# Kernel optimization log

Hardware: AMD Instinct MI355X
Metric: run time of the kernel (lower is better)

## Reference

```python
import jax, jax.numpy as jnp
import numpy as np
from jax import lax

LATENT = 128
CODEBOOK = 1024

def _conv(x, w, b):
    # NCHW conv, kernel OIHW, stride 1, padding 1 (same)
    y = lax.conv_general_dilated(x, w, (1, 1), ((1, 1), (1, 1)),
                                 dimension_numbers=('NCHW', 'OIHW', 'NCHW'))
    return y + b[None, :, None, None]

def _conv_transpose(x, w, b):
    # ConvTranspose2d(k=3, s=1, p=1) == conv with flipped kernel, in/out swapped, pad 1
    w_eff = jnp.flip(w, (2, 3)).transpose(1, 0, 2, 3)  # [Cin,Cout,3,3] -> [Cout,Cin,3,3]
    return _conv(x, w_eff, b)

def _maxpool2(x):
    return lax.reduce_window(x, -jnp.inf, lax.max, (1, 1, 2, 2), (1, 1, 2, 2), 'VALID')

def _upsample2(x):
    # F.interpolate(scale_factor=2), default nearest
    return jnp.repeat(jnp.repeat(x, 2, axis=2), 2, axis=3)

def setup_inputs() -> dict:
    key = jax.random.key(0)
    ks = jax.random.split(key, 20)
    f = jnp.float32
    inp = {
        'x': jax.random.uniform(ks[0], (8192, 1, 24, 24), dtype=f),
        'conv1_w': jax.random.normal(ks[1], (32, 1, 3, 3), f) * 0.1,
        'conv1_b': jnp.zeros((32,), f),
        'conv2_w': jax.random.normal(ks[2], (64, 32, 3, 3), f) * 0.05,
        'conv2_b': jnp.zeros((64,), f),
        'conv3_w': jax.random.normal(ks[3], (128, 64, 3, 3), f) * 0.04,
        'conv3_b': jnp.zeros((128,), f),
        'enc_fc_w': jax.random.normal(ks[4], (LATENT, 3 * 3 * 128), f) * 0.03,
        'enc_fc_b': jnp.zeros((LATENT,), f),
        'codebook': jax.random.normal(ks[5], (CODEBOOK, LATENT), f),
        'dec_fc_w': jax.random.normal(ks[6], (3 * 3 * 128, LATENT), f) * 0.09,
        'dec_fc_b': jnp.zeros((3 * 3 * 128,), f),
        'dct1_w': jax.random.normal(ks[7], (128, 64, 3, 3), f) * 0.03,  # [Cin,Cout,kh,kw]
        'dct1_b': jnp.zeros((64,), f),
        'dct2_w': jax.random.normal(ks[8], (64, 32, 3, 3), f) * 0.04,
        'dct2_b': jnp.zeros((32,), f),
        'dct3_w': jax.random.normal(ks[9], (32, 1, 3, 3), f) * 0.06,
        'dct3_b': jnp.zeros((1,), f),
    }
    return inp

def reference(x, conv1_w, conv1_b, conv2_w, conv2_b, conv3_w, conv3_b,
              enc_fc_w, enc_fc_b, codebook, dec_fc_w, dec_fc_b,
              dct1_w, dct1_b, dct2_w, dct2_b, dct3_w, dct3_b):
    # ---- Encoder ----
    h = _maxpool2(jax.nn.relu(_conv(x, conv1_w, conv1_b)))     # [B,32,12,12]
    h = _maxpool2(jax.nn.relu(_conv(h, conv2_w, conv2_b)))     # [B,64,6,6]
    h = _maxpool2(jax.nn.relu(_conv(h, conv3_w, conv3_b)))     # [B,128,3,3]
    z = h.reshape(-1, 3 * 3 * 128) @ enc_fc_w.T + enc_fc_b     # [B,128]
    # ---- Quantize (L2 nearest-codeword; matmul-trick distances, same argmin) ----
    d2 = (jnp.sum(z * z, axis=1, keepdims=True)
          - 2.0 * z @ codebook.T
          + jnp.sum(codebook * codebook, axis=1)[None, :])     # [B,K]
    idx = jnp.argmin(d2, axis=1)                               # [B]
    z_q = codebook[idx]                                        # [B,128]
    # ---- Decoder ----
    d = z_q @ dec_fc_w.T + dec_fc_b                            # [B,1152]
    d = d.reshape(-1, 128, 3, 3)
    d = _upsample2(jax.nn.relu(_conv_transpose(d, dct1_w, dct1_b)))  # [B,64,6,6]
    d = _upsample2(jax.nn.relu(_conv_transpose(d, dct2_w, dct2_b)))  # [B,32,12,12]
    d = _upsample2(jax.nn.relu(_conv_transpose(d, dct3_w, dct3_b)))  # [B,1,24,24]
    return d
```

## Files before the change

kernel.cpp:

```cpp
#include <hip/hip_runtime.h>

typedef __attribute__((ext_vector_type(8))) short short8;
typedef __attribute__((ext_vector_type(4))) float f32x4;
typedef unsigned short ushort_t;
typedef unsigned int uint_t;

#define OFF_W1R   0
#define OFF_BD2F  288
#define OFF_BD1F  18720
#define OFF_EWT   (18720+73728)
#define OFF_CT    (92448+147456)
#define OFF_CC    (239904+131072)
#define OFF_DWT   (370976+1024)
#define OFF_D1R   (372000+147456)
#define OFF_D3R   (593184+18432)
#define WS_WEIGHTS (611616+288)
#define OFF_W2BF  WS_WEIGHTS
#define OFF_W3BF  (OFF_W2BF+18432)
#define OFF_H     (OFF_W3BF+73728)
#define OFF_TABLE OFF_H
#define OFF_IDSN  (OFF_H+8192*1152)

__device__ __forceinline__ ushort_t f2bf(float v) {
  uint_t u = __float_as_uint(v);
  return (ushort_t)((u + 0x7FFFu + ((u >> 16) & 1u)) >> 16);
}
__device__ __forceinline__ float bf2f(ushort_t b) {
  return __uint_as_float(((uint_t)b) << 16);
}

#define P2_N (92160 + 294912 + 262144 + 73728 + 18432)
#define PREP_N (WS_WEIGHTS + P2_N)
__global__ void vq_prep_all(const float* __restrict__ conv1_w, const float* __restrict__ conv2_w,
                            const float* __restrict__ conv3_w, const float* __restrict__ enc_fc_w,
                            const float* __restrict__ codebook, const float* __restrict__ dec_fc_w,
                            const float* __restrict__ dct1_w, const float* __restrict__ dct2_w,
                            const float* __restrict__ dct3_w, float* __restrict__ ws) {
  int i0 = blockIdx.x * blockDim.x + threadIdx.x;
  if (i0 >= PREP_N) return;
  if (i0 < WS_WEIGHTS) {
    int i = i0;
    if (i < OFF_BD2F) {
      int tap = i >> 5, co = i & 31;
      ws[i] = conv1_w[co*9 + tap];
    } else if (i < OFF_CC) {
      return;
    } else if (i < OFF_DWT) {
      int k = i - OFF_CC;
      float s = 0.f;
      for (int j = 0; j < 128; ++j) { float v = codebook[k*128+j]; s += v*v; }
      ws[i] = s;
    } else if (i < OFF_D1R) {
      int l = i - OFF_DWT;
      int j = l % 1152, k = l / 1152;
      ws[i] = dec_fc_w[j*128 + k];
    } else if (i < OFF_D3R) {
      return;
    } else {
      int l = i - OFF_D3R;
      int tap = l % 9, ci = l / 9;
      ws[i] = dct3_w[ci*9 + (8 - tap)];
    }
    return;
  }
  int i = i0 - WS_WEIGHTS;
  ushort_t* W2  = (ushort_t*)(ws + OFF_W2BF);
  ushort_t* W3  = (ushort_t*)(ws + OFF_W3BF);
  ushort_t* EW  = (ushort_t*)(ws + OFF_EWT);
  ushort_t* CB  = (ushort_t*)(ws + OFF_CT);
  ushort_t* BD1 = (ushort_t*)(ws + OFF_BD1F);
  ushort_t* BD2 = (ushort_t*)(ws + OFF_BD2F);
  if (i < 18432) {
    int tap = i >> 11, r = i & 2047, co = r >> 5, ch = r & 31;
    float v = conv2_w[(co*32 + ch)*9 + tap];
    ushort_t hb = f2bf(v);
    W2[i] = hb; W2[18432 + i] = f2bf(v - bf2f(hb));
  } else if (i < 92160) {
    int j = i - 18432;
    int tap = j >> 13, r = j & 8191, co = r >> 6, ch = r & 63;
    float v = conv3_w[(co*64 + ch)*9 + tap];
    ushort_t hb = f2bf(v);
    W3[j] = hb; W3[73728 + j] = f2bf(v - bf2f(hb));
  } else if (i < 387072) {
    int r = i - 92160;
    int p = r / 147456; r %= 147456;
    int kk = r & 31, n = (r >> 5) & 127, ks = r >> 12;
    float v = enc_fc_w[n*1152 + ks*32 + kk];
    ushort_t hb = f2bf(v);
    if (p == 0) EW[r] = hb; else EW[147456 + r] = f2bf(v - bf2f(hb));
  } else if (i < 649216) {
    int r = i - 387072;
    int p = r / 131072; r %= 131072;
    int kk = r & 31, cw = (r >> 5) & 1023, ks = r >> 15;
    float v = codebook[cw*128 + ks*32 + kk];
    ushort_t hb = f2bf(v);
    if (p == 0) CB[r] = hb; else CB[131072 + r] = f2bf(v - bf2f(hb));
  } else if (i < 722944) {
    int r = i - 649216;
    int co = r / 1152, k = r - co*1152;
    int tap = k >> 7, ci = k & 127;
    float v = dct1_w[(ci*64 + co)*9 + (8 - tap)];
    ushort_t hb = f2bf(v);
    BD1[r] = hb; BD1[73728 + r] = f2bf(v - bf2f(hb));
  } else {
    int r = i - 722944;
    int co = r / 576, k = r - co*576;
    int tap = k >> 6, ci = k & 63;
    float v = dct2_w[(ci*32 + co)*9 + (8 - tap)];
    ushort_t hb = f2bf(v);
    BD2[r] = hb; BD2[18432 + r] = f2bf(v - bf2f(hb));
  }
}

__global__ __launch_bounds__(256, 4) void vq_enc(
    const float* __restrict__ x,
    const float* __restrict__ b1, const float* __restrict__ b2, const float* __restrict__ b3,
    const float* __restrict__ ws, ushort_t* __restrict__ hhi, ushort_t* __restrict__ hlo)
{
  __shared__ ushort_t R0h[7840], R0l[7840];
  __shared__ float XT[624];
  ushort_t* C3h = R0h;
  ushort_t* C3l = R0l;
  const int t = threadIdx.x;
  const int b = blockIdx.x;

  for (int i = t; i < 3920; i += 256) { ((uint_t*)R0h)[i] = 0u; ((uint_t*)R0l)[i] = 0u; }
  const float* xb = x + (size_t)b * 576;
  for (int i = t; i < 624; i += 256) {
    int row = i / 26, col = i - row * 26;
    XT[i] = (col >= 1 && col <= 24) ? xb[row*24 + col - 1] : 0.f;
  }
  __syncthreads();

  {
    int co = t & 31, g = t >> 5, gy = g >> 1, gx = g & 1;
    float w[9];
    #pragma unroll
    for (int k = 0; k < 9; ++k) w[k] = ws[OFF_W1R + k*32 + co];
    float bias = b1[co];
    #pragma unroll
    for (int pr = 0; pr < 3; ++pr) {
      int Y = gy*6 + pr*2;
      float a0[12], a1[12];
      #pragma unroll
      for (int i = 0; i < 12; ++i) { a0[i] = 0.f; a1[i] = 0.f; }
      #pragma unroll
      for (int wy = 0; wy < 4; ++wy) {
        int ry = Y - 1 + wy;
        if (ry < 0 || ry > 23) continue;
        const float2* rp = (const float2*)&XT[ry*26 + gx*12];
        float r[14];
        #pragma unroll
        for (int k = 0; k < 7; ++k) { float2 p = rp[k]; r[2*k] = p.x; r[2*k+1] = p.y; }
        if (wy < 3) {
          #pragma unroll
          for (int xx = 0; xx < 12; ++xx)
            #pragma unroll
            for (int dx = 0; dx < 3; ++dx) a0[xx] += r[xx+dx] * w[wy*3+dx];
        }
        if (wy >= 1) {
          #pragma unroll
          for (int xx = 0; xx < 12; ++xx)
            #pragma unroll
            for (int dx = 0; dx < 3; ++dx) a1[xx] += r[xx+dx] * w[(wy-1)*3+dx];
        }
      }
      #pragma unroll
      for (int pc = 0; pc < 6; ++pc) {
        float m = fmaxf(fmaxf(a0[2*pc], a0[2*pc+1]), fmaxf(a1[2*pc], a1[2*pc+1]));
        float v = m + bias; v = v > 0.f ? v : 0.f;
        int row = gy*3 + pr, colp = gx*6 + pc;
        int addr = ((row+1)*14 + (colp+1))*40 + co;
        ushort_t hb = f2bf(v);
        R0h[addr] = hb;
        R0l[addr] = f2bf(v - bf2f(hb));
      }
    }
  }
  __syncthreads();

  const int lane = t & 63, quad = lane >> 4, col = lane & 15;
  const int wv = t >> 6;

  {
    const int h = wv & 1, p = wv >> 1;
    const ushort_t* W2 = (const ushort_t*)(ws + OFF_W2BF);
    int baseA[5];
    #pragma unroll
    for (int mi = 0; mi < 5; ++mi) {
      int m = (h*5 + mi)*16 + col; if (m > 143) m = 143;
      int cell = m >> 2, sub = m & 3;
      int opy = cell / 6, opx = cell - opy*6;
      int y = 2*opy + (sub >> 1), xx = 2*opx + (sub & 1);
      baseA[mi] = (y*14 + xx)*40 + quad*8;
    }
    f32x4 acc[5][2];
    #pragma unroll
    for (int mi = 0; mi < 5; ++mi) { acc[mi][0] = (f32x4)0.f; acc[mi][1] = (f32x4)0.f; }
    const int co0 = p*32 + col, co1 = co0 + 16;
    #pragma unroll
    for (int t9 = 0; t9 < 9; ++t9) {
      const int TAPOFF = ((t9/3)*14 + (t9%3))*40;
      int bidx = t9*2048 + quad*8;
      short8 Bh0 = *(const short8*)(W2 + bidx + co0*32);
      short8 Bh1 = *(const short8*)(W2 + bidx + co1*32);
      short8 Bl0 = *(const short8*)(W2 + 18432 + bidx + co0*32);
      short8 Bl1 = *(const short8*)(W2 + 18432 + bidx + co1*32);
      #pragma unroll
      for (int mi = 0; mi < 5; ++mi) {
        int a = baseA[mi] + TAPOFF;
        short8 Ah = *(const short8*)(R0h + a);
        short8 Al = *(const short8*)(R0l + a);
        acc[mi][0] = __builtin_amdgcn_mfma_f32_16x16x32_bf16(Al, Bh0, acc[mi][0], 0, 0, 0);
        acc[mi][0] = __builtin_amdgcn_mfma_f32_16x16x32_bf16(Ah, Bl0, acc[mi][0], 0, 0, 0);
        acc[mi][0] = __builtin_amdgcn_mfma_f32_16x16x32_bf16(Ah, Bh0, acc[mi][0], 0, 0, 0);
        acc[mi][1] = __builtin_amdgcn_mfma_f32_16x16x32_bf16(Al, Bh1, acc[mi][1], 0, 0, 0);
        acc[mi][1] = __builtin_amdgcn_mfma_f32_16x16x32_bf16(Ah, Bl1, acc[mi][1], 0, 0, 0);
        acc[mi][1] = __builtin_amdgcn_mfma_f32_16x16x32_bf16(Ah, Bh1, acc[mi][1], 0, 0, 0);
      }
    }
    __syncthreads();
    for (int i = t; i < 2304; i += 256) { ((uint_t*)C3h)[i] = 0u; ((uint_t*)C3l)[i] = 0u; }
    __syncthreads();
    #pragma unroll
    for (int mi = 0; mi < 5; ++mi) {
      int cell = (h*5 + mi)*4 + quad;
      if (cell < 36) {
        int opy = cell / 6, opx = cell - opy*6;
        int wa = ((opy+1)*8 + (opx+1))*72;
        #pragma unroll
        for (int j = 0; j < 2; ++j) {
          int ch = j ? co1 : co0;
          f32x4 a = acc[mi][j];
          float v = fmaxf(fmaxf(a.x, a.y), fmaxf(a.z, a.w)) + b2[ch];
          v = v > 0.f ? v : 0.f;
          ushort_t hb = f2bf(v);
          C3h[wa + ch] = hb;
          C3l[wa + ch] = f2bf(v - bf2f(hb));
        }
      }
    }
  }
  __syncthreads();

  {
    const ushort_t* W3 = (const ushort_t*)(ws + OFF_W3BF);
    int baseA[3];
    #pragma unroll
    for (int mt = 0; mt < 3; ++mt) {
      int m = mt*16 + col; if (m > 35) m = 35;
      int cell = m >> 2, sub = m & 3;
      int opy = cell / 3, opx = cell - opy*3;
      int y = 2*opy + (sub >> 1), xx = 2*opx + (sub & 1);
      baseA[mt] = (y*8 + xx)*72 + quad*8;
    }
    f32x4 acc[3][2];
    #pragma unroll
    for (int mt = 0; mt < 3; ++mt) { acc[mt][0] = (f32x4)0.f; acc[mt][1] = (f32x4)0.f; }
    const int co0 = wv*16 + col, co1 = co0 + 64;
    #pragma unroll
    for (int ks = 0; ks < 18; ++ks) {
      const int t9 = ks >> 1, ch0 = (ks & 1)*32;
      const int TAPOFF = ((t9/3)*8 + (t9%3))*72;
      int bidx = t9*8192 + ch0 + quad*8;
      short8 Bh0 = *(const short8*)(W3 + bidx + co0*64);
      short8 Bh1 = *(const short8*)(W3 + bidx + co1*64);
      short8 Bl0 = *(const short8*)(W3 + 73728 + bidx + co0*64);
      short8 Bl1 = *(const short8*)(W3 + 73728 + bidx + co1*64);
      #pragma unroll
      for (int mt = 0; mt < 3; ++mt) {
        int a = baseA[mt] + TAPOFF + ch0;
        short8 Ah = *(const short8*)(C3h + a);
        short8 Al = *(const short8*)(C3l + a);
        acc[mt][0] = __builtin_amdgcn_mfma_f32_16x16x32_bf16(Al, Bh0, acc[mt][0], 0, 0, 0);
        acc[mt][0] = __builtin_amdgcn_mfma_f32_16x16x32_bf16(Ah, Bl0, acc[mt][0], 0, 0, 0);
        acc[mt][0] = __builtin_amdgcn_mfma_f32_16x16x32_bf16(Ah, Bh0, acc[mt][0], 0, 0, 0);
        acc[mt][1] = __builtin_amdgcn_mfma_f32_16x16x32_bf16(Al, Bh1, acc[mt][1], 0, 0, 0);
        acc[mt][1] = __builtin_amdgcn_mfma_f32_16x16x32_bf16(Ah, Bl1, acc[mt][1], 0, 0, 0);
        acc[mt][1] = __builtin_amdgcn_mfma_f32_16x16x32_bf16(Ah, Bh1, acc[mt][1], 0, 0, 0);
      }
    }
    ushort_t* hb_ = hhi + (size_t)b * 1152;
    ushort_t* lb_ = hlo + (size_t)b * 1152;
    #pragma unroll
    for (int mt = 0; mt < 3; ++mt) {
      int cell = mt*4 + quad;
      if (cell < 9) {
        #pragma unroll
        for (int j = 0; j < 2; ++j) {
          int ch = j ? co1 : co0;
          f32x4 a = acc[mt][j];
          float v = fmaxf(fmaxf(a.x, a.y), fmaxf(a.z, a.w)) + b3[ch];
          v = v > 0.f ? v : 0.f;
          ushort_t hb2 = f2bf(v);
          hb_[ch*9 + cell] = hb2;
          lb_[ch*9 + cell] = f2bf(v - bf2f(hb2));
        }
      }
    }
  }
}

__global__ __launch_bounds__(256, 4) void vq_fc_argmin(
    const float* __restrict__ efb, const float* __restrict__ ws,
    const ushort_t* __restrict__ hhi, const ushort_t* __restrict__ hlo,
    int* __restrict__ ids)
{
  __shared__ float ZL[16*132];
  __shared__ float WVs[64];
  __shared__ int   WIs[64];
  const int t = threadIdx.x;
  const int sb = blockIdx.x * 16;
  const int lane = t & 63, wv = t >> 6;
  const int col = lane & 15, quad = lane >> 4;

  const ushort_t* EW  = (const ushort_t*)(ws + OFF_EWT);
  const ushort_t* CBB = (const ushort_t*)(ws + OFF_CT);

  f32x4 acc0 = (f32x4)0.f, acc1 = (f32x4)0.f;
  const size_t hrow = (size_t)(sb + col) * 1152 + quad*8;
  #pragma unroll 4
  for (int ks = 0; ks < 36; ++ks) {
    short8 Ah = *(const short8*)(hhi + hrow + ks*32);
    short8 Al = *(const short8*)(hlo + hrow + ks*32);
    int n0 = wv*32 + col, n1 = n0 + 16;
    const ushort_t* bp0 = EW + (ks*128 + n0)*32 + quad*8;
    const ushort_t* bp1 = EW + (ks*128 + n1)*32 + quad*8;
    short8 Bh0 = *(const short8*)(bp0);
    short8 Bl0 = *(const short8*)(bp0 + 147456);
    short8 Bh1 = *(const short8*)(bp1);
    short8 Bl1 = *(const short8*)(bp1 + 147456);
    acc0 = __builtin_amdgcn_mfma_f32_16x16x32_bf16(Al, Bh0, acc0, 0, 0, 0);
    acc0 = __builtin_amdgcn_mfma_f32_16x16x32_bf16(Ah, Bl0, acc0, 0, 0, 0);
    acc0 = __builtin_amdgcn_mfma_f32_16x16x32_bf16(Ah, Bh0, acc0, 0, 0, 0);
    acc1 = __builtin_amdgcn_mfma_f32_16x16x32_bf16(Al, Bh1, acc1, 0, 0, 0);
    acc1 = __builtin_amdgcn_mfma_f32_16x16x32_bf16(Ah, Bl1, acc1, 0, 0, 0);
    acc1 = __builtin_amdgcn_mfma_f32_16x16x32_bf16(Ah, Bh1, acc1, 0, 0, 0);
  }
  {
    int n0 = wv*32 + col, n1 = n0 + 16;
    float bs0 = efb[n0], bs1 = efb[n1];
    #pragma unroll
    for (int r = 0; r < 4; ++r) {
      int m = quad*4 + r;
      ZL[m*132 + n0] = acc0[r] + bs0;
      ZL[m*132 + n1] = acc1[r] + bs1;
    }
  }
  __syncthreads();

  short8 zAh[4], zAl[4];
  #pragma unroll
  for (int ks = 0; ks < 4; ++ks) {
    const float* zp = &ZL[col*132 + ks*32 + quad*8];
    float4 z0 = *(const float4*)zp;
    float4 z1 = *(const float4*)(zp + 4);
    float zv[8] = {z0.x, z0.y, z0.z, z0.w, z1.x, z1.y, z1.z, z1.w};
    ushort_t ph[8], pl[8];
    #pragma unroll
    for (int e = 0; e < 8; ++e) {
      ushort_t hb = f2bf(zv[e]);
      ph[e] = hb; pl[e] = f2bf(zv[e] - bf2f(hb));
    }
    zAh[ks] = *(const short8*)ph;
    zAl[ks] = *(const short8*)pl;
  }

  float bestv[4]; int besti[4];
  #pragma unroll
  for (int r = 0; r < 4; ++r) { bestv[r] = 3.4e38f; besti[r] = 0; }
  for (int c4 = 0; c4 < 4; ++c4) {
    f32x4 dacc[4];
    #pragma unroll
    for (int nn = 0; nn < 4; ++nn) dacc[nn] = (f32x4)0.f;
    #pragma unroll
    for (int ks = 0; ks < 4; ++ks) {
      #pragma unroll
      for (int nn = 0; nn < 4; ++nn) {
        int cw = (wv*16 + c4*4 + nn)*16 + col;
        const ushort_t* bp = CBB + (size_t)(ks*1024 + cw)*32 + quad*8;
        short8 Bh = *(const short8*)bp;
        short8 Bl = *(const short8*)(bp + 131072);
        dacc[nn] = __builtin_amdgcn_mfma_f32_16x16x32_bf16(zAl[ks], Bh, dacc[nn], 0, 0, 0);
        dacc[nn] = __builtin_amdgcn_mfma_f32_16x16x32_bf16(zAh[ks], Bl, dacc[nn], 0, 0, 0);
        dacc[nn] = __builtin_amdgcn_mfma_f32_16x16x32_bf16(zAh[ks], Bh, dacc[nn], 0, 0, 0);
      }
    }
    #pragma unroll
    for (int nn = 0; nn < 4; ++nn) {
      int cw = (wv*16 + c4*4 + nn)*16 + col;
      float ccv = ws[OFF_CC + cw];
      #pragma unroll
      for (int r = 0; r < 4; ++r) {
        float dist = ccv - 2.f*dacc[nn][r];
        if (dist < bestv[r]) { bestv[r] = dist; besti[r] = cw; }
      }
    }
  }

  #pragma unroll
  for (int r = 0; r < 4; ++r) {
    float v = bestv[r]; int ii = besti[r];
    #pragma unroll
    for (int off = 8; off >= 1; off >>= 1) {
      float v2 = __shfl_xor(v, off); int i2 = __shfl_xor(ii, off);
      if (v2 < v || (v2 == v && i2 < ii)) { v = v2; ii = i2; }
    }
    if (col == 0) {
      int m = quad*4 + r;
      WVs[wv*16 + m] = v; WIs[wv*16 + m] = ii;
    }
  }
  __syncthreads();
  if (t < 16) {
    float v = WVs[t]; int ii = WIs[t];
    #pragma unroll
    for (int w2 = 1; w2 < 4; ++w2) {
      float v2 = WVs[w2*16 + t]; int i2 = WIs[w2*16 + t];
      if (v2 < v || (v2 == v && i2 < ii)) { v = v2; ii = i2; }
    }
    ids[sb + t] = ii;
  }
}

__global__ __launch_bounds__(256, 4) void vq_dec_table(
    const float* __restrict__ codebook, const float* __restrict__ decb,
    const float* __restrict__ d1b, const float* __restrict__ d2b, const float* __restrict__ d3b,
    const float* __restrict__ ws, float* __restrict__ table)
{
  __shared__ float POOL[8008];
  __shared__ float PS[1536];
  __shared__ float ZQ[128];
  ushort_t* FAh = (ushort_t*)POOL;
  ushort_t* FAl = FAh + 3400;
  ushort_t* GAh = (ushort_t*)(POOL + 3400);
  ushort_t* GAl = GAh + 4608;
  float* R2 = POOL;

  const int t = threadIdx.x;
  const int cw = blockIdx.x;
  const int lane = t & 63, wv = t >> 6;
  const int col = lane & 15, quad = lane >> 4;

  for (int i = t; i < 8008; i += 256) POOL[i] = 0.f;
  if (t < 128) ZQ[t] = codebook[(size_t)cw*128 + t];
  __syncthreads();

  #pragma unroll
  for (int p = 0; p < 5; ++p) {
    int j = t + p*256;
    if (j < 1152) {
      float a0 = decb[j];
      const float* wb = ws + OFF_DWT + j;
      #pragma unroll 4
      for (int k = 0; k < 128; ++k) a0 += wb[k*1152] * ZQ[k];
      int ci = j / 9, rem = j - ci*9;
      int pix = ((rem/3)+1)*5 + (rem%3) + 1;
      ushort_t hb = f2bf(a0);
      FAh[pix*136 + ci] = hb;
      FAl[pix*136 + ci] = f2bf(a0 - bf2f(hb));
    }
  }
  __syncthreads();

  const ushort_t* BD1 = (const ushort_t*)(ws + OFF_BD1F);
  f32x4 acc1 = (f32x4)0.f;
  {
    const int m9 = col < 9 ? col : 8;
    const int oy = m9/3, ox = m9 - oy*3;
    const int co = wv*16 + col;
    #pragma unroll 4
    for (int ks = 0; ks < 36; ++ks) {
      int kb = ks*32 + quad*8;
      int tap = kb >> 7, ci0 = kb & 127;
      int pix = (oy + tap/3)*5 + ox + tap%3;
      short8 Ah = *(const short8*)(FAh + pix*136 + ci0);
      short8 Al = *(const short8*)(FAl + pix*136 + ci0);
      const ushort_t* bp = BD1 + co*1152 + kb;
      short8 Bh = *(const short8*)bp;
      short8 Bl = *(const short8*)(bp + 73728);
      acc1 = __builtin_amdgcn_mfma_f32_16x16x32_bf16(Al, Bh, acc1, 0, 0, 0);
      acc1 = __builtin_amdgcn_mfma_f32_16x16x32_bf16(Ah, Bl, acc1, 0, 0, 0);
      acc1 = __builtin_amdgcn_mfma_f32_16x16x32_bf16(Ah, Bh, acc1, 0, 0, 0);
    }
  }
  {
    const int co = wv*16 + col;
    float bias = d1b[co];
    #pragma unroll
    for (int r = 0; r < 4; ++r) {
      int m = quad*4 + r;
      if (m < 9) {
        int oy = m/3, ox = m - oy*3;
        float v = acc1[r] + bias; v = v > 0.f ? v : 0.f;
        ushort_t hb = f2bf(v), lb = f2bf(v - bf2f(hb));
        int rbase = (2*oy+1)*8 + (2*ox+1);
        GAh[(rbase  )*72 + co] = hb; GAh[(rbase+1)*72 + co] = hb;
        GAh[(rbase+8)*72 + co] = hb; GAh[(rbase+9)*72 + co] = hb;
        GAl[(rbase  )*72 + co] = lb; GAl[(rbase+1)*72 + co] = lb;
        GAl[(rbase+8)*72 + co] = lb; GAl[(rbase+9)*72 + co] = lb;
      }
    }
  }
  __syncthreads();

  const ushort_t* BD2 = (const ushort_t*)(ws + OFF_BD2F);
  f32x4 acc2[3];
  acc2[0] = (f32x4)0.f; acc2[1] = (f32x4)0.f; acc2[2] = (f32x4)0.f;
  const int h = wv >> 1, js = (wv & 1)*3;
  for (int ks = h*9; ks < h*9 + 9; ++ks) {
    int kb = ks*32 + quad*8;
    int tap = kb >> 6, ci0 = kb & 63;
    int ty = tap/3, tx = tap - ty*3;
    #pragma unroll
    for (int jj = 0; jj < 3; ++jj) {
      int job = js + jj;
      int mt = job >> 1, nt = job & 1;
      int m = mt*16 + col; if (m > 35) m = 35;
      int oy = m/6, ox = m - oy*6;
      int pix = (oy+ty)*8 + ox+tx;
      short8 Ah = *(const short8*)(GAh + pix*72 + ci0);
      short8 Al = *(const short8*)(GAl + pix*72 + ci0);
      int co = nt*16 + col;
      const ushort_t* bp = BD2 + co*576 + kb;
      short8 Bh = *(const short8*)bp;
      short8 Bl = *(const short8*)(bp + 18432);
      acc2[jj] = __builtin_amdgcn_mfma_f32_16x16x32_bf16(Al, Bh, acc2[jj], 0, 0, 0);
      acc2[jj] = __builtin_amdgcn_mfma_f32_16x16x32_bf16(Ah, Bl, acc2[jj], 0, 0, 0);
      acc2[jj] = __builtin_amdgcn_mfma_f32_16x16x32_bf16(Ah, Bh, acc2[jj], 0, 0, 0);
    }
  }
  __syncthreads();
  if (h == 1) {
    #pragma unroll
    for (int jj = 0; jj < 3; ++jj) {
      int job = js + jj;
      #pragma unroll
      for (int r = 0; r < 4; ++r) PS[(job*64 + lane)*4 + r] = acc2[jj][r];
    }
  }
  for (int i = t; i < 6468; i += 256) R2[i] = 0.f;
  __syncthreads();
  if (h == 0) {
    #pragma unroll
    for (int jj = 0; jj < 3; ++jj) {
      int job = js + jj;
      int mt = job >> 1, nt = job & 1;
      int co = nt*16 + col;
      float bias = d2b[co];
      #pragma unroll
      for (int r = 0; r < 4; ++r) {
        float v = acc2[jj][r] + PS[(job*64 + lane)*4 + r];
        int m = mt*16 + quad*4 + r;
        if (m < 36) {
          int oy = m/6, ox = m - oy*6;
          v += bias; v = v > 0.f ? v : 0.f;
          int rbase = (2*oy+1)*14 + (2*ox+1);
          R2[(rbase   )*33 + co] = v; R2[(rbase+ 1)*33 + co] = v;
          R2[(rbase+14)*33 + co] = v; R2[(rbase+15)*33 + co] = v;
        }
      }
    }
  }
  __syncthreads();

  if (t < 144) {
    int yy = t / 12, xx = t - yy*12;
    const float* w3 = ws + OFF_D3R;
    float acc = d3b[0];
    #pragma unroll
    for (int dy = 0; dy < 3; ++dy)
      #pragma unroll
      for (int dx = 0; dx < 3; ++dx) {
        const float* rp = &R2[((yy+dy)*14 + xx+dx)*33];
        const float* wp = w3 + dy*3 + dx;
        #pragma unroll 8
        for (int ci = 0; ci < 32; ++ci) acc += rp[ci] * wp[ci*9];
      }
    float v = acc > 0.f ? acc : 0.f;
    float* ob = table + (size_t)cw * 576;
    int o0 = (2*yy)*24 + 2*xx;
    ob[o0] = v; ob[o0+1] = v; ob[o0+24] = v; ob[o0+25] = v;
  }
}

__global__ __launch_bounds__(256, 8) void vq_scatter(
    const float* __restrict__ table, const int* __restrict__ ids,
    float* __restrict__ out, int nvec)
{
  int idx = blockIdx.x * 256 + threadIdx.x;
  if (idx >= nvec) return;
  int b = idx / 144;
  int r = idx - b * 144;
  int cw = ids[b];
  ((float4*)out)[idx] = ((const float4*)(table + (size_t)cw * 576))[r];
}

extern "C" void kernel_launch(void* const* d_in, const int* in_sizes, int n_in,
                              void* d_out, int out_size, void* d_ws, size_t ws_size,
                              hipStream_t stream) {
  const float* x   = (const float*)d_in[0];
  const float* c1w = (const float*)d_in[1];
  const float* c1b = (const float*)d_in[2];
  const float* c2w = (const float*)d_in[3];
  const float* c2b = (const float*)d_in[4];
  const float* c3w = (const float*)d_in[5];
  const float* c3b = (const float*)d_in[6];
  const float* efw = (const float*)d_in[7];
  const float* efb = (const float*)d_in[8];
  const float* cb  = (const float*)d_in[9];
  const float* dfw = (const float*)d_in[10];
  const float* dfb = (const float*)d_in[11];
  const float* dw1 = (const float*)d_in[12];
  const float* db1 = (const float*)d_in[13];
  const float* dw2 = (const float*)d_in[14];
  const float* db2 = (const float*)d_in[15];
  const float* dw3 = (const float*)d_in[16];
  const float* db3 = (const float*)d_in[17];
  float* ws = (float*)d_ws;
  ushort_t* hhi  = (ushort_t*)(ws + OFF_H);
  ushort_t* hlo  = hhi + (size_t)8192*1152;
  float* table = ws + OFF_TABLE;
  int*   ids   = (int*)(ws + OFF_IDSN);
  float* outp = (float*)d_out;
  int B = in_sizes[0] / 576;

  vq_prep_all<<<(PREP_N + 255) / 256, 256, 0, stream>>>(c1w, c2w, c3w, efw, cb, dfw, dw1, dw2, dw3, ws);
  vq_enc<<<B, 256, 0, stream>>>(x, c1b, c2b, c3b, ws, hhi, hlo);
  vq_fc_argmin<<<B/16, 256, 0, stream>>>(efb, ws, hhi, hlo, ids);
  vq_dec_table<<<1024, 256, 0, stream>>>(cb, dfb, db1, db2, db3, ws, table);
  int nvec = B * 144;
  vq_scatter<<<(nvec + 255) / 256, 256, 0, stream>>>(table, ids, outp, nvec);
}
```

Baseline: 627.4 us.

## Fuse argmin with decoder-table scatter and retile conv2 MFMA across waves

The FC+argmin kernel and the scatter kernel are merged: each block computes codeword indices for its 16 samples and copies the matching decoded rows from the table straight to the output. This drops one launch and the ids round trip. It requires the table to get its own workspace region instead of aliasing the encoder activations. Separately, the conv2 MFMA tiling in the encoder is changed so each wave covers all 64 output channels with 2-3 M-tiles rather than 5 M-tiles by 32 channels. This cuts redundant A-fragment LDS loads but leaves the waves unevenly loaded.

```diff
diff --git a/kernel.cpp b/kernel.cpp
--- a/kernel.cpp
+++ b/kernel.cpp
@@ -18,8 +18,7 @@
 #define OFF_W2BF  WS_WEIGHTS
 #define OFF_W3BF  (OFF_W2BF+18432)
 #define OFF_H     (OFF_W3BF+73728)
-#define OFF_TABLE OFF_H
-#define OFF_IDSN  (OFF_H+8192*1152)
+#define OFF_TABLE (OFF_H + 8192*1152)
 
 __device__ __forceinline__ ushort_t f2bf(float v) {
   uint_t u = __float_as_uint(v);
@@ -183,55 +182,66 @@
   const int wv = t >> 6;
 
   {
-    const int h = wv & 1, p = wv >> 1;
     const ushort_t* W2 = (const ushort_t*)(ws + OFF_W2BF);
-    int baseA[5];
-    #pragma unroll
-    for (int mi = 0; mi < 5; ++mi) {
-      int m = (h*5 + mi)*16 + col; if (m > 143) m = 143;
+    const int cnt = (wv == 0) ? 3 : 2;
+    const int mtb = (wv == 0) ? 0 : 2*wv + 1;
+    int baseA[3];
+    #pragma unroll
+    for (int mi = 0; mi < 3; ++mi) {
+      int mt = mtb + (mi < cnt ? mi : cnt - 1);
+      int m = mt*16 + col;
       int cell = m >> 2, sub = m & 3;
       int opy = cell / 6, opx = cell - opy*6;
       int y = 2*opy + (sub >> 1), xx = 2*opx + (sub & 1);
       baseA[mi] = (y*14 + xx)*40 + quad*8;
     }
-    f32x4 acc[5][2];
-    #pragma unroll
-    for (int mi = 0; mi < 5; ++mi) { acc[mi][0] = (f32x4)0.f; acc[mi][1] = (f32x4)0.f; }
-    const int co0 = p*32 + col, co1 = co0 + 16;
+    f32x4 acc[3][4];
+    #pragma unroll
+    for (int mi = 0; mi < 3; ++mi)
+      #pragma unroll
+      for (int nt = 0; nt < 4; ++nt) acc[mi][nt] = (f32x4)0.f;
     #pragma unroll
     for (int t9 = 0; t9 < 9; ++t9) {
       const int TAPOFF = ((t9/3)*14 + (t9%3))*40;
+      short8 Ah[3], Al[3];
+      #pragma unroll
+      for (int mi = 0; mi < 3; ++mi) {
+        if (mi < cnt) {
+          int a = baseA[mi] + TAPOFF;
+          Ah[mi] = *(const short8*)(R0h + a);
+          Al[mi] = *(const short8*)(R0l + a);
+        }
+      }
       int bidx = t9*2048 + quad*8;
-      short8 Bh0 = *(const short8*)(W2 + bidx + co0*32);
-      short8 Bh1 = *(const short8*)(W2 + bidx + co1*32);
-      short8 Bl0 = *(const short8*)(W2 + 18432 + bidx + co0*32);
-      short8 Bl1 = *(const short8*)(W2 + 18432 + bidx + co1*32);
-      #pragma unroll
-      for (int mi = 0; mi < 5; ++mi) {
-        int a = baseA[mi] + TAPOFF;
-        short8 Ah = *(const short8*)(R0h + a);
-        short8 Al = *(const short8*)(R0l + a);
-        acc[mi][0] = __builtin_amdgcn_mfma_f32_16x16x32_bf16(Al, Bh0, acc[mi][0], 0, 0, 0);
-        acc[mi][0] = __builtin_amdgcn_mfma_f32_16x16x32_bf16(Ah, Bl0, acc[mi][0], 0, 0, 0);
-        acc[mi][0] = __builtin_amdgcn_mfma_f32_16x16x32_bf16(Ah, Bh0, acc[mi][0], 0, 0, 0);
-        acc[mi][1] = __builtin_amdgcn_mfma_f32_16x16x32_bf16(Al, Bh1, acc[mi][1], 0, 0, 0);
-        acc[mi][1] = __builtin_amdgcn_mfma_f32_16x16x32_bf16(Ah, Bl1, acc[mi][1], 0, 0, 0);
-        acc[mi][1] = __builtin_amdgcn_mfma_f32_16x16x32_bf16(Ah, Bh1, acc[mi][1], 0, 0, 0);
+      #pragma unroll
+      for (int nt = 0; nt < 4; ++nt) {
+        int co = nt*16 + col;
+        short8 Bh = *(const short8*)(W2 + bidx + co*32);
+        short8 Bl = *(const short8*)(W2 + 18432 + bidx + co*32);
+        #pragma unroll
+        for (int mi = 0; mi < 3; ++mi) {
+          if (mi < cnt) {
+            acc[mi][nt] = __builtin_amdgcn_mfma_f32_16x16x32_bf16(Al[mi], Bh, acc[mi][nt], 0, 0, 0);
+            acc[mi][nt] = __builtin_amdgcn_mfma_f32_16x16x32_bf16(Ah[mi], Bl, acc[mi][nt], 0, 0, 0);
+            acc[mi][nt] = __builtin_amdgcn_mfma_f32_16x16x32_bf16(Ah[mi], Bh, acc[mi][nt], 0, 0, 0);
+          }
+        }
       }
     }
     __syncthreads();
     for (int i = t; i < 2304; i += 256) { ((uint_t*)C3h)[i] = 0u; ((uint_t*)C3l)[i] = 0u; }
     __syncthreads();
     #pragma unroll
-    for (int mi = 0; mi < 5; ++mi) {
-      int cell = (h*5 + mi)*4 + quad;
-      if (cell < 36) {
+    for (int mi = 0; mi < 3; ++mi) {
+      if (mi < cnt) {
+        int mt = mtb + mi;
+        int cell = mt*4 + quad;
         int opy = cell / 6, opx = cell - opy*6;
         int wa = ((opy+1)*8 + (opx+1))*72;
         #pragma unroll
-        for (int j = 0; j < 2; ++j) {
-          int ch = j ? co1 : co0;
-          f32x4 a = acc[mi][j];
+        for (int nt = 0; nt < 4; ++nt) {
+          int ch = nt*16 + col;
+          f32x4 a = acc[mi][nt];
           float v = fmaxf(fmaxf(a.x, a.y), fmaxf(a.z, a.w)) + b2[ch];
           v = v > 0.f ? v : 0.f;
           ushort_t hb = f2bf(v);
@@ -298,128 +308,6 @@
         }
       }
     }
-  }
-}
-
-__global__ __launch_bounds__(256, 4) void vq_fc_argmin(
-    const float* __restrict__ efb, const float* __restrict__ ws,
-    const ushort_t* __restrict__ hhi, const ushort_t* __restrict__ hlo,
-    int* __restrict__ ids)
-{
-  __shared__ float ZL[16*132];
-  __shared__ float WVs[64];
-  __shared__ int   WIs[64];
-  const int t = threadIdx.x;
-  const int sb = blockIdx.x * 16;
-  const int lane = t & 63, wv = t >> 6;
-  const int col = lane & 15, quad = lane >> 4;
-
-  const ushort_t* EW  = (const ushort_t*)(ws + OFF_EWT);
-  const ushort_t* CBB = (const ushort_t*)(ws + OFF_CT);
-
-  f32x4 acc0 = (f32x4)0.f, acc1 = (f32x4)0.f;
-  const size_t hrow = (size_t)(sb + col) * 1152 + quad*8;
-  #pragma unroll 4
-  for (int ks = 0; ks < 36; ++ks) {
-    short8 Ah = *(const short8*)(hhi + hrow + ks*32);
-    short8 Al = *(const short8*)(hlo + hrow + ks*32);
-    int n0 = wv*32 + col, n1 = n0 + 16;
-    const ushort_t* bp0 = EW + (ks*128 + n0)*32 + quad*8;
-    const ushort_t* bp1 = EW + (ks*128 + n1)*32 + quad*8;
-    short8 Bh0 = *(const short8*)(bp0);
-    short8 Bl0 = *(const short8*)(bp0 + 147456);
-    short8 Bh1 = *(const short8*)(bp1);
-    short8 Bl1 = *(const short8*)(bp1 + 147456);
-    acc0 = __builtin_amdgcn_mfma_f32_16x16x32_bf16(Al, Bh0, acc0, 0, 0, 0);
-    acc0 = __builtin_amdgcn_mfma_f32_16x16x32_bf16(Ah, Bl0, acc0, 0, 0, 0);
-    acc0 = __builtin_amdgcn_mfma_f32_16x16x32_bf16(Ah, Bh0, acc0, 0, 0, 0);
-    acc1 = __builtin_amdgcn_mfma_f32_16x16x32_bf16(Al, Bh1, acc1, 0, 0, 0);
-    acc1 = __builtin_amdgcn_mfma_f32_16x16x32_bf16(Ah, Bl1, acc1, 0, 0, 0);
-    acc1 = __builtin_amdgcn_mfma_f32_16x16x32_bf16(Ah, Bh1, acc1, 0, 0, 0);
-  }
-  {
-    int n0 = wv*32 + col, n1 = n0 + 16;
-    float bs0 = efb[n0], bs1 = efb[n1];
-    #pragma unroll
-    for (int r = 0; r < 4; ++r) {
-      int m = quad*4 + r;
-      ZL[m*132 + n0] = acc0[r] + bs0;
-      ZL[m*132 + n1] = acc1[r] + bs1;
-    }
-  }
-  __syncthreads();
-
-  short8 zAh[4], zAl[4];
-  #pragma unroll
-  for (int ks = 0; ks < 4; ++ks) {
-    const float* zp = &ZL[col*132 + ks*32 + quad*8];
-    float4 z0 = *(const float4*)zp;
-    float4 z1 = *(const float4*)(zp + 4);
-    float zv[8] = {z0.x, z0.y, z0.z, z0.w, z1.x, z1.y, z1.z, z1.w};
-    ushort_t ph[8], pl[8];
-    #pragma unroll
-    for (int e = 0; e < 8; ++e) {
-      ushort_t hb = f2bf(zv[e]);
-      ph[e] = hb; pl[e] = f2bf(zv[e] - bf2f(hb));
-    }
-    zAh[ks] = *(const short8*)ph;
-    zAl[ks] = *(const short8*)pl;
-  }
-
-  float bestv[4]; int besti[4];
-  #pragma unroll
-  for (int r = 0; r < 4; ++r) { bestv[r] = 3.4e38f; besti[r] = 0; }
-  for (int c4 = 0; c4 < 4; ++c4) {
-    f32x4 dacc[4];
-    #pragma unroll
-    for (int nn = 0; nn < 4; ++nn) dacc[nn] = (f32x4)0.f;
-    #pragma unroll
-    for (int ks = 0; ks < 4; ++ks) {
-      #pragma unroll
-      for (int nn = 0; nn < 4; ++nn) {
-        int cw = (wv*16 + c4*4 + nn)*16 + col;
-        const ushort_t* bp = CBB + (size_t)(ks*1024 + cw)*32 + quad*8;
-        short8 Bh = *(const short8*)bp;
-        short8 Bl = *(const short8*)(bp + 131072);
-        dacc[nn] = __builtin_amdgcn_mfma_f32_16x16x32_bf16(zAl[ks], Bh, dacc[nn], 0, 0, 0);
-        dacc[nn] = __builtin_amdgcn_mfma_f32_16x16x32_bf16(zAh[ks], Bl, dacc[nn], 0, 0, 0);
-        dacc[nn] = __builtin_amdgcn_mfma_f32_16x16x32_bf16(zAh[ks], Bh, dacc[nn], 0, 0, 0);
-      }
-    }
-    #pragma unroll
-    for (int nn = 0; nn < 4; ++nn) {
-      int cw = (wv*16 + c4*4 + nn)*16 + col;
-      float ccv = ws[OFF_CC + cw];
-      #pragma unroll
-      for (int r = 0; r < 4; ++r) {
-        float dist = ccv - 2.f*dacc[nn][r];
-        if (dist < bestv[r]) { bestv[r] = dist; besti[r] = cw; }
-      }
-    }
-  }
-
-  #pragma unroll
-  for (int r = 0; r < 4; ++r) {
-    float v = bestv[r]; int ii = besti[r];
-    #pragma unroll
-    for (int off = 8; off >= 1; off >>= 1) {
-      float v2 = __shfl_xor(v, off); int i2 = __shfl_xor(ii, off);
-      if (v2 < v || (v2 == v && i2 < ii)) { v = v2; ii = i2; }
-    }
-    if (col == 0) {
-      int m = quad*4 + r;
-      WVs[wv*16 + m] = v; WIs[wv*16 + m] = ii;
-    }
-  }
-  __syncthreads();
-  if (t < 16) {
-    float v = WVs[t]; int ii = WIs[t];
-    #pragma unroll
-    for (int w2 = 1; w2 < 4; ++w2) {
-      float v2 = WVs[w2*16 + t]; int i2 = WIs[w2*16 + t];
-      if (v2 < v || (v2 == v && i2 < ii)) { v = v2; ii = i2; }
-    }
-    ids[sb + t] = ii;
   }
 }
 
@@ -584,16 +472,134 @@
   }
 }
 
-__global__ __launch_bounds__(256, 8) void vq_scatter(
-    const float* __restrict__ table, const int* __restrict__ ids,
-    float* __restrict__ out, int nvec)
+__global__ __launch_bounds__(256, 4) void vq_fc_argmin_scatter(
+    const float* __restrict__ efb, const float* __restrict__ ws,
+    const ushort_t* __restrict__ hhi, const ushort_t* __restrict__ hlo,
+    const float* __restrict__ table, float* __restrict__ out)
 {
-  int idx = blockIdx.x * 256 + threadIdx.x;
-  if (idx >= nvec) return;
-  int b = idx / 144;
-  int r = idx - b * 144;
-  int cw = ids[b];
-  ((float4*)out)[idx] = ((const float4*)(table + (size_t)cw * 576))[r];
+  __shared__ float ZL[16*132];
+  __shared__ float WVs[64];
+  __shared__ int   WIs[64];
+  __shared__ int   IDX[16];
+  const int t = threadIdx.x;
+  const int sb = blockIdx.x * 16;
+  const int lane = t & 63, wv = t >> 6;
+  const int col = lane & 15, quad = lane >> 4;
+
+  const ushort_t* EW  = (const ushort_t*)(ws + OFF_EWT);
+  const ushort_t* CBB = (const ushort_t*)(ws + OFF_CT);
+
+  f32x4 acc0 = (f32x4)0.f, acc1 = (f32x4)0.f;
+  const size_t hrow = (size_t)(sb + col) * 1152 + quad*8;
+  const int n0 = wv*32 + col, n1 = n0 + 16;
+  #pragma unroll 4
+  for (int ks = 0; ks < 36; ++ks) {
+    short8 Ah = *(const short8*)(hhi + hrow + ks*32);
+    short8 Al = *(const short8*)(hlo + hrow + ks*32);
+    const ushort_t* bp0 = EW + (ks*128 + n0)*32 + quad*8;
+    const ushort_t* bp1 = EW + (ks*128 + n1)*32 + quad*8;
+    short8 Bh0 = *(const short8*)(bp0);
+    short8 Bl0 = *(const short8*)(bp0 + 147456);
+    short8 Bh1 = *(const short8*)(bp1);
+    short8 Bl1 = *(const short8*)(bp1 + 147456);
+    acc0 = __builtin_amdgcn_mfma_f32_16x16x32_bf16(Al, Bh0, acc0, 0, 0, 0);
+    acc0 = __builtin_amdgcn_mfma_f32_16x16x32_bf16(Ah, Bl0, acc0, 0, 0, 0);
+    acc0 = __builtin_amdgcn_mfma_f32_16x16x32_bf16(Ah, Bh0, acc0, 0, 0, 0);
+    acc1 = __builtin_amdgcn_mfma_f32_16x16x32_bf16(Al, Bh1, acc1, 0, 0, 0);
+    acc1 = __builtin_amdgcn_mfma_f32_16x16x32_bf16(Ah, Bl1, acc1, 0, 0, 0);
+    acc1 = __builtin_amdgcn_mfma_f32_16x16x32_bf16(Ah, Bh1, acc1, 0, 0, 0);
+  }
+  {
+    float bs0 = efb[n0], bs1 = efb[n1];
+    #pragma unroll
+    for (int r = 0; r < 4; ++r) {
+      int m = quad*4 + r;
+      ZL[m*132 + n0] = acc0[r] + bs0;
+      ZL[m*132 + n1] = acc1[r] + bs1;
+    }
+  }
+  __syncthreads();
+
+  short8 zAh[4], zAl[4];
+  #pragma unroll
+  for (int ks = 0; ks < 4; ++ks) {
+    const float* zp = &ZL[col*132 + ks*32 + quad*8];
+    float4 z0 = *(const float4*)zp;
+    float4 z1 = *(const float4*)(zp + 4);
+    float zv[8] = {z0.x, z0.y, z0.z, z0.w, z1.x, z1.y, z1.z, z1.w};
+    ushort_t ph[8], pl[8];
+    #pragma unroll
+    for (int e = 0; e < 8; ++e) {
+      ushort_t hb = f2bf(zv[e]);
+      ph[e] = hb; pl[e] = f2bf(zv[e] - bf2f(hb));
+    }
+    zAh[ks] = *(const short8*)ph;
+    zAl[ks] = *(const short8*)pl;
+  }
+
+  float bestv[4]; int besti[4];
+  #pragma unroll
+  for (int r = 0; r < 4; ++r) { bestv[r] = 3.4e38f; besti[r] = 0; }
+  for (int c4 = 0; c4 < 4; ++c4) {
+    f32x4 dacc[4];
+    #pragma unroll
+    for (int nn = 0; nn < 4; ++nn) dacc[nn] = (f32x4)0.f;
+    #pragma unroll
+    for (int ks = 0; ks < 4; ++ks) {
+      #pragma unroll
+      for (int nn = 0; nn < 4; ++nn) {
+        int cw = (wv*16 + c4*4 + nn)*16 + col;
+        const ushort_t* bp = CBB + (size_t)(ks*1024 + cw)*32 + quad*8;
+        short8 Bh = *(const short8*)bp;
+        short8 Bl = *(const short8*)(bp + 131072);
+        dacc[nn] = __builtin_amdgcn_mfma_f32_16x16x32_bf16(zAl[ks], Bh, dacc[nn], 0, 0, 0);
+        dacc[nn] = __builtin_amdgcn_mfma_f32_16x16x32_bf16(zAh[ks], Bl, dacc[nn], 0, 0, 0);
+        dacc[nn] = __builtin_amdgcn_mfma_f32_16x16x32_bf16(zAh[ks], Bh, dacc[nn], 0, 0, 0);
+      }
+    }
+    #pragma unroll
+    for (int nn = 0; nn < 4; ++nn) {
+      int cw = (wv*16 + c4*4 + nn)*16 + col;
+      float ccv = ws[OFF_CC + cw];
+      #pragma unroll
+      for (int r = 0; r < 4; ++r) {
+        float dist = ccv - 2.f*dacc[nn][r];
+        if (dist < bestv[r]) { bestv[r] = dist; besti[r] = cw; }
+      }
+    }
+  }
+
+  #pragma unroll
+  for (int r = 0; r < 4; ++r) {
+    float v = bestv[r]; int ii = besti[r];
+    #pragma unroll
+    for (int off = 8; off >= 1; off >>= 1) {
+      float v2 = __shfl_xor(v, off); int i2 = __shfl_xor(ii, off);
+      if (v2 < v || (v2 == v && i2 < ii)) { v = v2; ii = i2; }
+    }
+    if (col == 0) {
+      int m = quad*4 + r;
+      WVs[wv*16 + m] = v; WIs[wv*16 + m] = ii;
+    }
+  }
+  __syncthreads();
+  if (t < 16) {
+    float v = WVs[t]; int ii = WIs[t];
+    #pragma unroll
+    for (int w2 = 1; w2 < 4; ++w2) {
+      float v2 = WVs[w2*16 + t]; int i2 = WIs[w2*16 + t];
+      if (v2 < v || (v2 == v && i2 < ii)) { v = v2; ii = i2; }
+    }
+    IDX[t] = ii;
+  }
+  __syncthreads();
+
+  const float4* tb4 = (const float4*)table;
+  float4* out4 = (float4*)(out + (size_t)sb * 576);
+  for (int i = t; i < 16*144; i += 256) {
+    int s = i / 144, r = i - s*144;
+    out4[s*144 + r] = tb4[(size_t)IDX[s]*144 + r];
+  }
 }
 
 extern "C" void kernel_launch(void* const* d_in, const int* in_sizes, int n_in,
@@ -621,14 +627,11 @@
   ushort_t* hhi  = (ushort_t*)(ws + OFF_H);
   ushort_t* hlo  = hhi + (size_t)8192*1152;
   float* table = ws + OFF_TABLE;
-  int*   ids   = (int*)(ws + OFF_IDSN);
   float* outp = (float*)d_out;
   int B = in_sizes[0] / 576;
 
   vq_prep_all<<<(PREP_N + 255) / 256, 256, 0, stream>>>(c1w, c2w, c3w, efw, cb, dfw, dw1, dw2, dw3, ws);
   vq_enc<<<B, 256, 0, stream>>>(x, c1b, c2b, c3b, ws, hhi, hlo);
-  vq_fc_argmin<<<B/16, 256, 0, stream>>>(efb, ws, hhi, hlo, ids);
   vq_dec_table<<<1024, 256, 0, stream>>>(cb, dfb, db1, db2, db3, ws, table);
-  int nvec = B * 144;
-  vq_scatter<<<(nvec + 255) / 256, 256, 0, stream>>>(table, ids, outp, nvec);
+  vq_fc_argmin_scatter<<<B/16, 256, 0, stream>>>(efb, ws, hhi, hlo, table, outp);
 }
```

New measurement: 679.0 us. 1.08x slower.
